# Kernel optimization log

Hardware: AMD Instinct MI355X
Metric: run time of the kernel (lower is better)

## Reference

```python
import jax, jax.numpy as jnp
import numpy as np

N_NODES = 2048   # n_nodes; also ChebConv in/out channels (feature dim F == N)
C = 2            # n_data_per_node
K = 2            # cheby_kernel_size
E = 65536        # number of edges (avg degree 32)


def setup_inputs() -> dict:
    key = jax.random.key(0)
    k0, k1, k2, k3, k4 = jax.random.split(key, 5)
    x = jax.random.normal(k0, (N_NODES, C, N_NODES), dtype=jnp.float32)
    edge_index = jax.random.randint(k1, (2, E), 0, N_NODES)
    edge_weight = jax.random.uniform(k2, (E,), dtype=jnp.float32)
    # Stacked ChebConv params: one (K, F_in, F_out) Theta and (F_out,) bias per (i, j) pair.
    W = jax.random.normal(k3, (C, C, K, N_NODES, N_NODES), dtype=jnp.float32) * 0.02
    b = jax.random.normal(k4, (C, C, N_NODES), dtype=jnp.float32) * 0.02
    return {"x": x, "edge_index": edge_index, "edge_weight": edge_weight, "W": W, "b": b}


def _cheb_norm(edge_index, edge_weight, n):
    # PyG ChebConv normalization with normalization='sym', lambda_max=2.0:
    # L_hat = (2/lmax)*(I - D^-1/2 A D^-1/2) - I = -D^-1/2 A D^-1/2 (diagonal term is 0).
    row, col = edge_index[0], edge_index[1]
    deg = jnp.zeros((n,), edge_weight.dtype).at[row].add(edge_weight)
    safe = jnp.where(deg > 0, deg, 1.0)
    dis = jnp.where(deg > 0, jax.lax.rsqrt(safe), 0.0)
    return -dis[row] * edge_weight * dis[col]


def _propagate(x, row, col, w):
    # x: (B, N, C, F). Gather from source nodes (row), scatter-add into target nodes (col).
    msg = w[None, :, None, None] * x[:, row]          # (B, E, C, F)
    return jnp.zeros_like(x).at[:, col].add(msg)


def reference(x, edge_index, edge_weight, W, b):
    x_ = x[None]                                      # (1, N, C, F), F == N
    row, col = edge_index[0], edge_index[1]
    w = _cheb_norm(edge_index, edge_weight, x.shape[0])
    # Chebyshev recursion, shared across all input channels j simultaneously.
    Tx0 = x_
    Tx1 = _propagate(Tx0, row, col, w)
    Txs = [Tx0, Tx1]
    for _ in range(2, K):
        Txs.append(2.0 * _propagate(Txs[-1], row, col, w) - Txs[-2])
    Txs = jnp.stack(Txs)                              # (K, B, N, C, F)
    # y[:, :, i, :] = relu( sum_j ( sum_k Tx_k[..., j, :] @ W[i, j, k] + b[i, j] ) )
    y = jnp.einsum('kbnjf,ijkfg->bnig', Txs, W) + jnp.sum(b, axis=1)
    return jax.nn.relu(y)                             # (1, N, C, F)
```

## Files before the change

### kernel.cpp

```cpp
#include <hip/hip_runtime.h>

#define N_NODES 2048
#define EDGES   65536

typedef __bf16 bf16x8 __attribute__((ext_vector_type(8)));
typedef float  f32x4  __attribute__((ext_vector_type(4)));

__device__ __forceinline__ unsigned short f2bf(float f) {
  unsigned u = __builtin_bit_cast(unsigned, f);
  unsigned r = u + 0x7FFFu + ((u >> 16) & 1u);
  return (unsigned short)(r >> 16);
}
__device__ __forceinline__ float bf2f(unsigned short h) {
  return __builtin_bit_cast(float, (unsigned)h << 16);
}
__device__ __forceinline__ void split1(float f, unsigned short& hi, unsigned short& lo) {
  hi = f2bf(f);
  lo = f2bf(f - bf2f(hi));
}

__global__ void k_deg(const int* __restrict__ ei, const float* __restrict__ ew,
                      float* __restrict__ deg) {
  int e = blockIdx.x * 256 + threadIdx.x;
  atomicAdd(&deg[ei[e]], ew[e]);
}
__global__ void k_dis(const float* __restrict__ deg, float* __restrict__ dis) {
  int n = blockIdx.x * 256 + threadIdx.x;
  float d = deg[n];
  dis[n] = d > 0.f ? 1.f / sqrtf(d) : 0.f;
}
__global__ void k_scatterS(const int* __restrict__ ei, const float* __restrict__ ew,
                           const float* __restrict__ dis, float* __restrict__ S) {
  int e = blockIdx.x * 256 + threadIdx.x;
  int r = ei[e], c = ei[EDGES + e];
  float w = -dis[r] * ew[e] * dis[c];
  atomicAdd(&S[c * N_NODES + r], w);
}
__global__ void k_bsum(const float* __restrict__ b, float* __restrict__ bs) {
  int t = blockIdx.x * 256 + threadIdx.x;
  int i = t >> 11, g = t & 2047;
  bs[t] = b[(i * 2 + 0) * 2048 + g] + b[(i * 2 + 1) * 2048 + g];
}

template <int MODE>
__global__ __launch_bounds__(256, 2)
void gemm_split(const float* __restrict__ A0, const float* __restrict__ A1,
                const float* __restrict__ Bsrc, const float* __restrict__ bias,
                float* __restrict__ Cout, int Kdim) {
  __shared__ unsigned short As_hi[128 * 32];
  __shared__ unsigned short As_lo[128 * 32];
  __shared__ unsigned short Bs_hi[128 * 32];
  __shared__ unsigned short Bs_lo[128 * 32];

  const int tid  = threadIdx.x;
  const int lane = tid & 63;
  const int wid  = tid >> 6;
  const int wr   = wid >> 1, wc = wid & 1;
  const int n0   = blockIdx.x * 128;
  const int m0   = blockIdx.y * 128;

  const int lda = (MODE == 0) ? 2048 : 4096;
  const int ldb = (MODE == 0) ? 4096 : 2048;

  const int a_m  = tid >> 3;
  const int a_k4 = tid & 7;
  const int b_n4 = tid & 31;
  const int b_kg = tid >> 5;

  const int awb = a_m * 64 + (((8 * a_k4) & 48) ^ ((a_m & 3) << 4)) + ((8 * a_k4) & 8);
  const int bwb = (4 * b_n4) * 64 + (((8 * b_kg) & 48) ^ ((b_n4 & 3) << 4)) + ((8 * b_kg) & 8);

  int arb[4], brb[4];
#pragma unroll
  for (int mf = 0; mf < 4; ++mf) {
    int row = wr * 64 + mf * 16 + (lane & 15);
    arb[mf] = row * 64 + ((((lane >> 4) << 4)) ^ ((lane & 3) << 4));
  }
#pragma unroll
  for (int nf = 0; nf < 4; ++nf) {
    int row = wc * 64 + nf * 16 + (lane & 15);
    brb[nf] = row * 64 + ((((lane >> 4) << 4)) ^ (((lane >> 2) & 3) << 4));
  }

  f32x4 acc[4][4] = {};

  for (int k0 = 0; k0 < Kdim; k0 += 32) {
    const float* Ab;
    if (MODE == 0) Ab = A0 + k0;
    else           Ab = (k0 < 4096) ? (A0 + k0) : (A1 + (k0 - 4096));
    const float* Bb;
    if (MODE == 0) {
      Bb = Bsrc + (size_t)k0 * 4096 + n0;
    } else {
      int kjb = k0 >> 11;
      int ii  = n0 >> 11;
      int f0  = k0 & 2047, g0 = n0 & 2047;
      int jj  = kjb & 1, kc = kjb >> 1;
      Bb = Bsrc + ((size_t)((ii * 2 + jj) * 2 + kc) << 22) + (size_t)f0 * 2048 + g0;
    }

    __syncthreads();

#pragma unroll
    for (int p = 0; p < 4; ++p) {
      int m = a_m + p * 32;
      const float4 v = *(const float4*)(Ab + (size_t)(m0 + m) * lda + a_k4 * 4);
      ushort4 hi, lo;
      split1(v.x, hi.x, lo.x);
      split1(v.y, hi.y, lo.y);
      split1(v.z, hi.z, lo.z);
      split1(v.w, hi.w, lo.w);
      int byte = awb + p * 2048;
      *(ushort4*)((char*)As_hi + byte) = hi;
      *(ushort4*)((char*)As_lo + byte) = lo;
    }

    {
      const float* bp = Bb + (size_t)(b_kg * 4) * ldb + b_n4 * 4;
      const float4 r0 = *(const float4*)(bp);
      const float4 r1 = *(const float4*)(bp + ldb);
      const float4 r2 = *(const float4*)(bp + 2 * (size_t)ldb);
      const float4 r3 = *(const float4*)(bp + 3 * (size_t)ldb);
      const float c0[4] = {r0.x, r1.x, r2.x, r3.x};
      const float c1[4] = {r0.y, r1.y, r2.y, r3.y};
      const float c2[4] = {r0.z, r1.z, r2.z, r3.z};
      const float c3[4] = {r0.w, r1.w, r2.w, r3.w};
      const float* cols[4] = {c0, c1, c2, c3};
#pragma unroll
      for (int c = 0; c < 4; ++c) {
        ushort4 hi, lo;
        split1(cols[c][0], hi.x, lo.x);
        split1(cols[c][1], hi.y, lo.y);
        split1(cols[c][2], hi.z, lo.z);
        split1(cols[c][3], hi.w, lo.w);
        int byte = bwb + c * 64;
        *(ushort4*)((char*)Bs_hi + byte) = hi;
        *(ushort4*)((char*)Bs_lo + byte) = lo;
      }
    }

    __syncthreads();

    bf16x8 ah[4], al[4], bh[4], bl[4];
#pragma unroll
    for (int mf = 0; mf < 4; ++mf) {
      ah[mf] = *(const bf16x8*)((const char*)As_hi + arb[mf]);
      al[mf] = *(const bf16x8*)((const char*)As_lo + arb[mf]);
    }
#pragma unroll
    for (int nf = 0; nf < 4; ++nf) {
      bh[nf] = *(const bf16x8*)((const char*)Bs_hi + brb[nf]);
      bl[nf] = *(const bf16x8*)((const char*)Bs_lo + brb[nf]);
    }
#pragma unroll
    for (int mf = 0; mf < 4; ++mf) {
#pragma unroll
      for (int nf = 0; nf < 4; ++nf) {
        acc[mf][nf] = __builtin_amdgcn_mfma_f32_16x16x32_bf16(ah[mf], bh[nf], acc[mf][nf], 0, 0, 0);
        acc[mf][nf] = __builtin_amdgcn_mfma_f32_16x16x32_bf16(ah[mf], bl[nf], acc[mf][nf], 0, 0, 0);
        acc[mf][nf] = __builtin_amdgcn_mfma_f32_16x16x32_bf16(al[mf], bh[nf], acc[mf][nf], 0, 0, 0);
      }
    }
  }

#pragma unroll
  for (int mf = 0; mf < 4; ++mf) {
#pragma unroll
    for (int nf = 0; nf < 4; ++nf) {
      int col = n0 + wc * 64 + nf * 16 + (lane & 15);
      float bv = (MODE == 1) ? bias[col] : 0.f;
#pragma unroll
      for (int r = 0; r < 4; ++r) {
        int row = m0 + wr * 64 + mf * 16 + ((lane >> 4) * 4) + r;
        float v = acc[mf][nf][r] + bv;
        if (MODE == 1) v = fmaxf(v, 0.f);
        Cout[(size_t)row * 4096 + col] = v;
      }
    }
  }
}

extern "C" void kernel_launch(void* const* d_in, const int* in_sizes, int n_in,
                              void* d_out, int out_size, void* d_ws, size_t ws_size,
                              hipStream_t stream) {
  const float* x  = (const float*)d_in[0];
  const int*   ei = (const int*)d_in[1];
  const float* ew = (const float*)d_in[2];
  const float* W  = (const float*)d_in[3];
  const float* b  = (const float*)d_in[4];
  float* out = (float*)d_out;

  char* ws = (char*)d_ws;
  float* S    = (float*)(ws);
  float* deg  = (float*)(ws + 16777216);
  float* dis  = (float*)(ws + 16785408);
  float* bsum = (float*)(ws + 16793600);
  float* Tx1  = (float*)(ws + 16809984);

  hipMemsetAsync(S, 0, 16785408, stream);

  k_deg<<<EDGES / 256, 256, 0, stream>>>(ei, ew, deg);
  k_dis<<<N_NODES / 256, 256, 0, stream>>>(deg, dis);
  k_scatterS<<<EDGES / 256, 256, 0, stream>>>(ei, ew, dis, S);
  k_bsum<<<4096 / 256, 256, 0, stream>>>(b, bsum);

  dim3 grid(32, 16);
  gemm_split<0><<<grid, 256, 0, stream>>>(S, nullptr, x, nullptr, Tx1, 2048);
  gemm_split<1><<<grid, 256, 0, stream>>>(x, Tx1, W, bsum, out, 8192);
}
```

Baseline: 942.3 us.

## Pre-split operands to bf16 hi/lo and stream tiles via global_load_lds

Adds pre-pass kernels that split x, S and W into bf16 hi/lo planes, transposing x and W so both GEMM operands are K-contiguous. The GEMMs then copy tiles straight into LDS with global_load_lds and no longer convert in-loop. The first GEMM writes its output already split, and block indices are swizzled for L2 locality. This removes repeated per-tile fp32-to-bf16 conversion and register staging, at the cost of extra passes over the 128MB W tensor and larger workspace traffic.

```diff
diff --git a/kernel.cpp b/kernel.cpp
--- a/kernel.cpp
+++ b/kernel.cpp
@@ -5,6 +5,13 @@
 
 typedef __bf16 bf16x8 __attribute__((ext_vector_type(8)));
 typedef float  f32x4  __attribute__((ext_vector_type(4)));
+
+typedef __attribute__((address_space(1))) const unsigned int gu32;
+typedef __attribute__((address_space(3))) unsigned int lu32;
+
+__device__ __forceinline__ void gll16(const void* g, void* l) {
+  __builtin_amdgcn_global_load_lds((gu32*)g, (lu32*)l, 16, 0, 0);
+}
 
 __device__ __forceinline__ unsigned short f2bf(float f) {
   unsigned u = __builtin_bit_cast(unsigned, f);
@@ -42,115 +49,140 @@
   bs[t] = b[(i * 2 + 0) * 2048 + g] + b[(i * 2 + 1) * 2048 + g];
 }
 
+__global__ void k_split(const float* __restrict__ in, unsigned short* __restrict__ hi,
+                        unsigned short* __restrict__ lo) {
+  int t = blockIdx.x * 256 + threadIdx.x;
+  float4 v = ((const float4*)in)[t];
+  ushort4 h, l;
+  split1(v.x, h.x, l.x);
+  split1(v.y, h.y, l.y);
+  split1(v.z, h.z, l.z);
+  split1(v.w, h.w, l.w);
+  ((ushort4*)hi)[t] = h;
+  ((ushort4*)lo)[t] = l;
+}
+
+template <int WMODE>
+__global__ void k_tsplit(const float* __restrict__ in, unsigned short* __restrict__ oh,
+                         unsigned short* __restrict__ ol) {
+  __shared__ float tl[64][65];
+  const int tid = threadIdx.x;
+  int in_stride, out_stride;
+  size_t in_base, out_base;
+  if (WMODE == 0) {
+    in_stride = 4096; out_stride = 2048; in_base = 0; out_base = 0;
+  } else {
+    in_stride = 2048; out_stride = 8192;
+    int z = blockIdx.z;
+    int i = z >> 2, j = (z >> 1) & 1, k = z & 1;
+    in_base = (size_t)z << 22;
+    out_base = (size_t)i * 2048 * 8192 + (size_t)(k * 2 + j) * 2048;
+  }
+  const int r0 = blockIdx.y * 64, c0 = blockIdx.x * 64;
+
+#pragma unroll
+  for (int q = 0; q < 4; ++q) {
+    int s = q * 256 + tid;
+    int row = s >> 4, c4 = (s & 15) * 4;
+    float4 v = *(const float4*)(in + in_base + (size_t)(r0 + row) * in_stride + c0 + c4);
+    tl[row][c4 + 0] = v.x; tl[row][c4 + 1] = v.y;
+    tl[row][c4 + 2] = v.z; tl[row][c4 + 3] = v.w;
+  }
+  __syncthreads();
+#pragma unroll
+  for (int q = 0; q < 4; ++q) {
+    int s = q * 256 + tid;
+    int cc = s >> 4, rr = (s & 15) * 4;
+    ushort4 h, l;
+    split1(tl[rr + 0][cc], h.x, l.x);
+    split1(tl[rr + 1][cc], h.y, l.y);
+    split1(tl[rr + 2][cc], h.z, l.z);
+    split1(tl[rr + 3][cc], h.w, l.w);
+    size_t o = out_base + (size_t)(c0 + cc) * out_stride + r0 + rr;
+    *(ushort4*)(oh + o) = h;
+    *(ushort4*)(ol + o) = l;
+  }
+}
+
 template <int MODE>
 __global__ __launch_bounds__(256, 2)
-void gemm_split(const float* __restrict__ A0, const float* __restrict__ A1,
-                const float* __restrict__ Bsrc, const float* __restrict__ bias,
-                float* __restrict__ Cout, int Kdim) {
-  __shared__ unsigned short As_hi[128 * 32];
-  __shared__ unsigned short As_lo[128 * 32];
-  __shared__ unsigned short Bs_hi[128 * 32];
-  __shared__ unsigned short Bs_lo[128 * 32];
+void gemm_bf16(const unsigned short* __restrict__ Ah0, const unsigned short* __restrict__ Al0,
+               const unsigned short* __restrict__ Ah1, const unsigned short* __restrict__ Al1,
+               const unsigned short* __restrict__ Bh, const unsigned short* __restrict__ Bl,
+               const float* __restrict__ bias,
+               float* __restrict__ outF, unsigned short* __restrict__ outH,
+               unsigned short* __restrict__ outL, int Kdim) {
+  __shared__ unsigned short lds[4 * 4096];
 
   const int tid  = threadIdx.x;
   const int lane = tid & 63;
   const int wid  = tid >> 6;
   const int wr   = wid >> 1, wc = wid & 1;
-  const int n0   = blockIdx.x * 128;
-  const int m0   = blockIdx.y * 128;
-
-  const int lda = (MODE == 0) ? 2048 : 4096;
-  const int ldb = (MODE == 0) ? 4096 : 2048;
-
-  const int a_m  = tid >> 3;
-  const int a_k4 = tid & 7;
-  const int b_n4 = tid & 31;
-  const int b_kg = tid >> 5;
-
-  const int awb = a_m * 64 + (((8 * a_k4) & 48) ^ ((a_m & 3) << 4)) + ((8 * a_k4) & 8);
-  const int bwb = (4 * b_n4) * 64 + (((8 * b_kg) & 48) ^ ((b_n4 & 3) << 4)) + ((8 * b_kg) & 8);
+
+  const int flat = blockIdx.y * 32 + blockIdx.x;
+  const int swz  = (flat & 7) * 64 + (flat >> 3);
+  const int n0   = (swz & 31) * 128;
+  const int m0   = (swz >> 5) * 128;
+
+  const int ldab = ((MODE == 0) ? 2048 : 4096) * 2;
+  const int ldbb = ((MODE == 0) ? 2048 : 8192) * 2;
+
+  const int srow = wid * 32 + (lane >> 2);
+  const int kcl  = ((lane & 3) ^ ((lane >> 3) & 3)) * 16;
+  const size_t rowA = (size_t)(m0 + srow) * ldab + kcl;
+  const size_t rowB = (size_t)(n0 + srow) * ldbb + kcl;
+  const int ldsc = wid * 2048;
 
   int arb[4], brb[4];
-#pragma unroll
-  for (int mf = 0; mf < 4; ++mf) {
-    int row = wr * 64 + mf * 16 + (lane & 15);
-    arb[mf] = row * 64 + ((((lane >> 4) << 4)) ^ ((lane & 3) << 4));
-  }
-#pragma unroll
-  for (int nf = 0; nf < 4; ++nf) {
-    int row = wc * 64 + nf * 16 + (lane & 15);
-    brb[nf] = row * 64 + ((((lane >> 4) << 4)) ^ (((lane >> 2) & 3) << 4));
-  }
+  const int physr = ((lane >> 4) ^ ((lane >> 1) & 3)) * 16;
+#pragma unroll
+  for (int mf = 0; mf < 4; ++mf)
+    arb[mf] = (wr * 64 + mf * 16 + (lane & 15)) * 64 + physr;
+#pragma unroll
+  for (int nf = 0; nf < 4; ++nf)
+    brb[nf] = (wc * 64 + nf * 16 + (lane & 15)) * 64 + physr;
+
+  char* ldsb = (char*)lds;
 
   f32x4 acc[4][4] = {};
 
   for (int k0 = 0; k0 < Kdim; k0 += 32) {
-    const float* Ab;
-    if (MODE == 0) Ab = A0 + k0;
-    else           Ab = (k0 < 4096) ? (A0 + k0) : (A1 + (k0 - 4096));
-    const float* Bb;
-    if (MODE == 0) {
-      Bb = Bsrc + (size_t)k0 * 4096 + n0;
+    const char* bAh;
+    const char* bAl;
+    int kk = k0;
+    if (MODE == 1 && k0 >= 4096) {
+      bAh = (const char*)Ah1; bAl = (const char*)Al1; kk = k0 - 4096;
     } else {
-      int kjb = k0 >> 11;
-      int ii  = n0 >> 11;
-      int f0  = k0 & 2047, g0 = n0 & 2047;
-      int jj  = kjb & 1, kc = kjb >> 1;
-      Bb = Bsrc + ((size_t)((ii * 2 + jj) * 2 + kc) << 22) + (size_t)f0 * 2048 + g0;
-    }
+      bAh = (const char*)Ah0; bAl = (const char*)Al0;
+    }
+    const size_t ka = rowA + (size_t)kk * 2;
+    const size_t kb = rowB + (size_t)k0 * 2;
+    const char* bBh = (const char*)Bh;
+    const char* bBl = (const char*)Bl;
 
     __syncthreads();
-
-#pragma unroll
-    for (int p = 0; p < 4; ++p) {
-      int m = a_m + p * 32;
-      const float4 v = *(const float4*)(Ab + (size_t)(m0 + m) * lda + a_k4 * 4);
-      ushort4 hi, lo;
-      split1(v.x, hi.x, lo.x);
-      split1(v.y, hi.y, lo.y);
-      split1(v.z, hi.z, lo.z);
-      split1(v.w, hi.w, lo.w);
-      int byte = awb + p * 2048;
-      *(ushort4*)((char*)As_hi + byte) = hi;
-      *(ushort4*)((char*)As_lo + byte) = lo;
-    }
-
-    {
-      const float* bp = Bb + (size_t)(b_kg * 4) * ldb + b_n4 * 4;
-      const float4 r0 = *(const float4*)(bp);
-      const float4 r1 = *(const float4*)(bp + ldb);
-      const float4 r2 = *(const float4*)(bp + 2 * (size_t)ldb);
-      const float4 r3 = *(const float4*)(bp + 3 * (size_t)ldb);
-      const float c0[4] = {r0.x, r1.x, r2.x, r3.x};
-      const float c1[4] = {r0.y, r1.y, r2.y, r3.y};
-      const float c2[4] = {r0.z, r1.z, r2.z, r3.z};
-      const float c3[4] = {r0.w, r1.w, r2.w, r3.w};
-      const float* cols[4] = {c0, c1, c2, c3};
-#pragma unroll
-      for (int c = 0; c < 4; ++c) {
-        ushort4 hi, lo;
-        split1(cols[c][0], hi.x, lo.x);
-        split1(cols[c][1], hi.y, lo.y);
-        split1(cols[c][2], hi.z, lo.z);
-        split1(cols[c][3], hi.w, lo.w);
-        int byte = bwb + c * 64;
-        *(ushort4*)((char*)Bs_hi + byte) = hi;
-        *(ushort4*)((char*)Bs_lo + byte) = lo;
-      }
-    }
-
+#pragma unroll
+    for (int q = 0; q < 2; ++q) {
+      const size_t ra = ka + (size_t)q * 16 * ldab;
+      const size_t rb = kb + (size_t)q * 16 * ldbb;
+      const int dst = ldsc + q * 1024;
+      gll16(bAh + ra, ldsb + 0 * 8192 + dst);
+      gll16(bAl + ra, ldsb + 1 * 8192 + dst);
+      gll16(bBh + rb, ldsb + 2 * 8192 + dst);
+      gll16(bBl + rb, ldsb + 3 * 8192 + dst);
+    }
     __syncthreads();
 
     bf16x8 ah[4], al[4], bh[4], bl[4];
 #pragma unroll
     for (int mf = 0; mf < 4; ++mf) {
-      ah[mf] = *(const bf16x8*)((const char*)As_hi + arb[mf]);
-      al[mf] = *(const bf16x8*)((const char*)As_lo + arb[mf]);
+      ah[mf] = *(const bf16x8*)(ldsb + 0 * 8192 + arb[mf]);
+      al[mf] = *(const bf16x8*)(ldsb + 1 * 8192 + arb[mf]);
     }
 #pragma unroll
     for (int nf = 0; nf < 4; ++nf) {
-      bh[nf] = *(const bf16x8*)((const char*)Bs_hi + brb[nf]);
-      bl[nf] = *(const bf16x8*)((const char*)Bs_lo + brb[nf]);
+      bh[nf] = *(const bf16x8*)(ldsb + 2 * 8192 + brb[nf]);
+      bl[nf] = *(const bf16x8*)(ldsb + 3 * 8192 + brb[nf]);
     }
 #pragma unroll
     for (int mf = 0; mf < 4; ++mf) {
@@ -172,9 +204,16 @@
 #pragma unroll
       for (int r = 0; r < 4; ++r) {
         int row = m0 + wr * 64 + mf * 16 + ((lane >> 4) * 4) + r;
-        float v = acc[mf][nf][r] + bv;
-        if (MODE == 1) v = fmaxf(v, 0.f);
-        Cout[(size_t)row * 4096 + col] = v;
+        size_t o = (size_t)row * 4096 + col;
+        float v = acc[mf][nf][r];
+        if (MODE == 1) {
+          outF[o] = fmaxf(v + bv, 0.f);
+        } else {
+          unsigned short h, l;
+          split1(v, h, l);
+          outH[o] = h;
+          outL[o] = l;
+        }
       }
     }
   }
@@ -191,20 +230,41 @@
   float* out = (float*)d_out;
 
   char* ws = (char*)d_ws;
-  float* S    = (float*)(ws);
-  float* deg  = (float*)(ws + 16777216);
-  float* dis  = (float*)(ws + 16785408);
-  float* bsum = (float*)(ws + 16793600);
-  float* Tx1  = (float*)(ws + 16809984);
-
-  hipMemsetAsync(S, 0, 16785408, stream);
+  float*          S     = (float*)(ws + 0);
+  unsigned short* xT_hi = (unsigned short*)(ws + 16777216);
+  unsigned short* xT_lo = (unsigned short*)(ws + 33554432);
+  unsigned short* S_hi  = (unsigned short*)(ws + 50331648);
+  unsigned short* S_lo  = (unsigned short*)(ws + 58720256);
+  unsigned short* Wt_hi = (unsigned short*)(ws + 0);
+  unsigned short* Wt_lo = (unsigned short*)(ws + 67108864);
+  unsigned short* x_hi  = (unsigned short*)(ws + 134217728);
+  unsigned short* x_lo  = (unsigned short*)(ws + 150994944);
+  unsigned short* T_hi  = (unsigned short*)(ws + 167772160);
+  unsigned short* T_lo  = (unsigned short*)(ws + 184549376);
+  float*          deg   = (float*)(ws + 201326592);
+  float*          dis   = (float*)(ws + 201334784);
+  float*          bsum  = (float*)(ws + 201342976);
+
+  hipMemsetAsync(S, 0, 16777216, stream);
+  hipMemsetAsync(deg, 0, 8192, stream);
 
   k_deg<<<EDGES / 256, 256, 0, stream>>>(ei, ew, deg);
   k_dis<<<N_NODES / 256, 256, 0, stream>>>(deg, dis);
   k_scatterS<<<EDGES / 256, 256, 0, stream>>>(ei, ew, dis, S);
   k_bsum<<<4096 / 256, 256, 0, stream>>>(b, bsum);
 
+  k_split<<<2097152 / 256, 256, 0, stream>>>(x, x_hi, x_lo);
+  k_split<<<1048576 / 256, 256, 0, stream>>>(S, S_hi, S_lo);
+  k_tsplit<0><<<dim3(64, 32, 1), 256, 0, stream>>>(x, xT_hi, xT_lo);
+
   dim3 grid(32, 16);
-  gemm_split<0><<<grid, 256, 0, stream>>>(S, nullptr, x, nullptr, Tx1, 2048);
-  gemm_split<1><<<grid, 256, 0, stream>>>(x, Tx1, W, bsum, out, 8192);
-}
+  gemm_bf16<0><<<grid, 256, 0, stream>>>(S_hi, S_lo, nullptr, nullptr,
+                                         xT_hi, xT_lo, nullptr,
+                                         nullptr, T_hi, T_lo, 2048);
+
+  k_tsplit<1><<<dim3(32, 32, 8), 256, 0, stream>>>(W, Wt_hi, Wt_lo);
+
+  gemm_bf16<1><<<grid, 256, 0, stream>>>(x_hi, x_lo, T_hi, T_lo,
+                                         Wt_hi, Wt_lo, bsum,
+                                         out, nullptr, nullptr, 8192);
+}
```

After: 908.8 us. 3.6% less time.
